# Kernel optimization log

Hardware: AMD Instinct MI355X
Metric: run time of the kernel (lower is better)

## Reference

```python
import jax, jax.numpy as jnp
import numpy as np

N, C, T, V = 64, 64, 256, 25
H, O = 8, 64

def setup_inputs() -> dict:
    key = jax.random.key(0)
    ks = jax.random.split(key, 6)
    s = 0.05
    return {
        "x": jax.random.normal(ks[0], (N, C, T, V), dtype=jnp.float32),
        "A": jax.random.normal(ks[1], (V, V), dtype=jnp.float32) * 0.1,
        "alpha": jnp.float32(1.0),
        "Wq": jax.random.normal(ks[2], (H, C), dtype=jnp.float32) * s,
        "bq": jnp.zeros((H,), dtype=jnp.float32),
        "Wk": jax.random.normal(ks[3], (H, C), dtype=jnp.float32) * s,
        "bk": jnp.zeros((H,), dtype=jnp.float32),
        "Wv": jax.random.normal(ks[4], (O, C), dtype=jnp.float32) * s,
        "bv": jnp.zeros((O,), dtype=jnp.float32),
        "Wr": jax.random.normal(ks[5], (O, H), dtype=jnp.float32) * s,
        "br": jnp.zeros((O,), dtype=jnp.float32),
    }

def reference(x, A, alpha, Wq, bq, Wk, bk, Wv, bv, Wr, br):
    # 1x1 conv projections + temporal mean pooling (bias commutes with mean)
    t = x.shape[2]
    x_mean = x.mean(axis=2)                                   # (N, C, V)
    q = jnp.einsum('ncv,hc->nhv', x_mean, Wq) + bq[None, :, None]   # (N, H, V)
    k = jnp.einsum('ncv,hc->nhv', x_mean, Wk) + bk[None, :, None]   # (N, H, V)
    v = jnp.einsum('nctv,oc->notv', x, Wv) + bv[None, :, None, None]  # (N, O, T, V)
    # outer-difference tanh attention: (N, H, V, V)
    attn = jnp.tanh(q[:, :, :, None] - k[:, :, None, :])
    # 1x1 conv reproject heads -> out channels: (N, O, V, V)
    rep = jnp.einsum('nhuv,oh->nouv', attn, Wr) + br[None, :, None, None]
    masked = alpha * rep + A[None, None, :, :]
    # adjacency-weighted node aggregation
    out = jnp.einsum('ncuv,nctv->nctu', masked, v)            # (N, O, T, V)
    return out
```

## Files before the change

### kernel.cpp

```cpp
#include <hip/hip_runtime.h>
#include <hip/hip_bf16.h>

#define NB 64
#define CC 64
#define TT 256
#define VV 25
#define HH 8
#define OO 64
#define TV (TT*VV)
#define UV (VV*VV)
#define NCHUNK 25

__global__ __launch_bounds__(256) void k_prep(const float* __restrict__ Wv,
                                              float* __restrict__ WvT) {
    int i = blockIdx.x * 256 + threadIdx.x;
    int o = i >> 6, c = i & 63;
    WvT[c * OO + o] = Wv[o * CC + c];
}

__global__ __launch_bounds__(256) void k_vmean(const float* __restrict__ x,
                                               const float* __restrict__ WvT,
                                               const float* __restrict__ bv,
                                               float* __restrict__ vv,
                                               float* __restrict__ xpart) {
    int blk = blockIdx.x;
    int n = blk / NCHUNK, ch = blk % NCHUNK;
    int tid = threadIdx.x;
    int tv = ch * 256 + tid;
    int vloc = tv % VV;

    __shared__ float xacc[CC * VV];
    for (int i = tid; i < CC * VV; i += 256) xacc[i] = 0.0f;
    __syncthreads();

    const float*  xs  = x + (size_t)n * CC * TV + tv;
    const float2* W2  = (const float2*)WvT;
    const float2* bv2 = (const float2*)bv;

    float2 acc[OO / 2];
#pragma unroll
    for (int j = 0; j < OO / 2; ++j) acc[j] = bv2[j];

#pragma unroll 2
    for (int c = 0; c < CC; ++c) {
        float xv = xs[(size_t)c * TV];
        atomicAdd(&xacc[c * VV + vloc], xv);
#pragma unroll
        for (int j = 0; j < OO / 2; ++j) {
            float2 w = W2[c * (OO / 2) + j];
            acc[j].x += w.x * xv;
            acc[j].y += w.y * xv;
        }
    }

    float* dst = vv + (size_t)n * OO * TV + tv;
#pragma unroll
    for (int j = 0; j < OO / 2; ++j) {
        dst[(size_t)(2 * j) * TV]     = acc[j].x;
        dst[(size_t)(2 * j + 1) * TV] = acc[j].y;
    }

    __syncthreads();
    float* xg = xpart + (size_t)blk * (CC * VV);
    for (int i = tid; i < CC * VV; i += 256) xg[i] = xacc[i];
}

__global__ __launch_bounds__(256) void k_masked(
        float* __restrict__ buf,
        const float* __restrict__ A,
        const float* __restrict__ alpha_p,
        const float* __restrict__ Wq, const float* __restrict__ bq,
        const float* __restrict__ Wk, const float* __restrict__ bk,
        const float* __restrict__ Wr, const float* __restrict__ br) {
    int n = blockIdx.x, tid = threadIdx.x;
    __shared__ float xm[CC * VV];
    __shared__ float qs[HH * VV];
    __shared__ float ks[HH * VV];
    __shared__ float attn[HH * UV];

    const float* xp = buf + (size_t)n * (NCHUNK * CC * VV);
    for (int i = tid; i < CC * VV; i += 256) {
        float s = 0.0f;
#pragma unroll
        for (int ch = 0; ch < NCHUNK; ++ch) s += xp[ch * (CC * VV) + i];
        xm[i] = s * (1.0f / TT);
    }
    __syncthreads();

    for (int i = tid; i < 2 * HH * VV; i += 256) {
        int isK = i >= HH * VV;
        int hv = isK ? i - HH * VV : i;
        int h = hv / VV, v = hv % VV;
        const float* W = isK ? Wk : Wq;
        float s = isK ? bk[h] : bq[h];
        for (int c = 0; c < CC; ++c) s += xm[c * VV + v] * W[h * CC + c];
        if (isK) ks[hv] = s; else qs[hv] = s;
    }
    __syncthreads();

    for (int i = tid; i < HH * UV; i += 256) {
        int h = i / UV, uv = i % UV, u = uv / VV, v = uv % VV;
        attn[i] = tanhf(qs[h * VV + u] - ks[h * VV + v]);
    }
    __syncthreads();

    float alpha = alpha_p[0];
    float* mout = buf + (size_t)n * (OO * UV);
    for (int i = tid; i < OO * UV; i += 256) {
        int o = i / UV, uv = i % UV;
        float r = br[o];
#pragma unroll
        for (int h = 0; h < HH; ++h) r += Wr[o * HH + h] * attn[h * UV + uv];
        mout[i] = alpha * r + A[uv];
    }
}

__global__ __launch_bounds__(256) void k_aggr(float* __restrict__ io,
                                              const float* __restrict__ masked) {
    int no = blockIdx.x;
    int t  = threadIdx.x;
    __shared__ float buf[TV];
    float4* b4 = (float4*)buf;
    float4* g4 = (float4*)(io + (size_t)no * TV);

    for (int i = t; i < TV / 4; i += 256) b4[i] = g4[i];
    __syncthreads();

    float xv[VV];
#pragma unroll
    for (int v = 0; v < VV; ++v) xv[v] = buf[t * VV + v];

    const float* m = masked + (size_t)no * UV;
    float outr[VV];
#pragma unroll
    for (int u = 0; u < VV; ++u) {
        float a = 0.0f;
#pragma unroll
        for (int v = 0; v < VV; ++v) a += m[u * VV + v] * xv[v];
        outr[u] = a;
    }
#pragma unroll
    for (int u = 0; u < VV; ++u) buf[t * VV + u] = outr[u];
    __syncthreads();

    for (int i = t; i < TV / 4; i += 256) g4[i] = b4[i];
}

extern "C" void kernel_launch(void* const* d_in, const int* in_sizes, int n_in,
                              void* d_out, int out_size, void* d_ws, size_t ws_size,
                              hipStream_t stream) {
    const float* x     = (const float*)d_in[0];
    const float* A     = (const float*)d_in[1];
    const float* alpha = (const float*)d_in[2];
    const float* Wq    = (const float*)d_in[3];
    const float* bq    = (const float*)d_in[4];
    const float* Wk    = (const float*)d_in[5];
    const float* bk    = (const float*)d_in[6];
    const float* Wv    = (const float*)d_in[7];
    const float* bv    = (const float*)d_in[8];
    const float* Wr    = (const float*)d_in[9];
    const float* br    = (const float*)d_in[10];
    float* out = (float*)d_out;

    float* ws     = (float*)d_ws;
    float* xpart  = ws;
    float* masked = ws;
    float* WvT    = ws + (size_t)NB * OO * UV;

    k_prep  <<<(CC * OO) / 256, 256, 0, stream>>>(Wv, WvT);
    k_vmean <<<NB * NCHUNK, 256, 0, stream>>>(x, WvT, bv, out, xpart);
    k_masked<<<NB, 256, 0, stream>>>(masked, A, alpha, Wq, bq, Wk, bk, Wr, br);
    k_aggr  <<<NB * OO, 256, 0, stream>>>(out, masked);
}
```

Before: 396.6 us.

## Split temporal mean out of V projection into separate reduction kernel

Removes the per-element shared-memory atomicAdd that computed the temporal mean inside the V projection kernel, and puts that mean into its own kernel that reduces each (n,c) slab through shared memory. The V projection now processes four channels per iteration with float4 weight loads and sets a launch-bounds occupancy hint. The cost is a second full read of x (about 105MB) in exchange for cutting LDS atomic contention and the 25-chunk partial-sum buffer.

```diff
diff --git a/kernel.cpp b/kernel.cpp
--- a/kernel.cpp
+++ b/kernel.cpp
@@ -9,7 +9,6 @@
 #define OO 64
 #define TV (TT*VV)
 #define UV (VV*VV)
-#define NCHUNK 25
 
 __global__ __launch_bounds__(256) void k_prep(const float* __restrict__ Wv,
                                               float* __restrict__ WvT) {
@@ -18,73 +17,94 @@
     WvT[c * OO + o] = Wv[o * CC + c];
 }
 
-__global__ __launch_bounds__(256) void k_vmean(const float* __restrict__ x,
-                                               const float* __restrict__ WvT,
-                                               const float* __restrict__ bv,
-                                               float* __restrict__ vv,
-                                               float* __restrict__ xpart) {
+__global__ __launch_bounds__(256, 4) void k_vproj(const float* __restrict__ x,
+                                                  const float* __restrict__ WvT,
+                                                  const float* __restrict__ bv,
+                                                  float* __restrict__ vv) {
     int blk = blockIdx.x;
-    int n = blk / NCHUNK, ch = blk % NCHUNK;
-    int tid = threadIdx.x;
-    int tv = ch * 256 + tid;
-    int vloc = tv % VV;
+    int n = blk / 25, ch = blk % 25;
+    int tv = ch * 256 + threadIdx.x;
 
-    __shared__ float xacc[CC * VV];
-    for (int i = tid; i < CC * VV; i += 256) xacc[i] = 0.0f;
-    __syncthreads();
+    const float*  xs = x + (size_t)n * CC * TV + tv;
+    const float4* W4 = (const float4*)WvT;
+    const float4* b4 = (const float4*)bv;
 
-    const float*  xs  = x + (size_t)n * CC * TV + tv;
-    const float2* W2  = (const float2*)WvT;
-    const float2* bv2 = (const float2*)bv;
+    float4 a[OO / 4];
+#pragma unroll
+    for (int j = 0; j < OO / 4; ++j) a[j] = b4[j];
 
-    float2 acc[OO / 2];
+    for (int c = 0; c < CC; c += 4) {
+        float x0 = xs[(size_t)(c + 0) * TV];
+        float x1 = xs[(size_t)(c + 1) * TV];
+        float x2 = xs[(size_t)(c + 2) * TV];
+        float x3 = xs[(size_t)(c + 3) * TV];
 #pragma unroll
-    for (int j = 0; j < OO / 2; ++j) acc[j] = bv2[j];
-
-#pragma unroll 2
-    for (int c = 0; c < CC; ++c) {
-        float xv = xs[(size_t)c * TV];
-        atomicAdd(&xacc[c * VV + vloc], xv);
-#pragma unroll
-        for (int j = 0; j < OO / 2; ++j) {
-            float2 w = W2[c * (OO / 2) + j];
-            acc[j].x += w.x * xv;
-            acc[j].y += w.y * xv;
+        for (int j = 0; j < OO / 4; ++j) {
+            float4 w0 = W4[(c + 0) * (OO / 4) + j];
+            float4 w1 = W4[(c + 1) * (OO / 4) + j];
+            float4 w2 = W4[(c + 2) * (OO / 4) + j];
+            float4 w3 = W4[(c + 3) * (OO / 4) + j];
+            a[j].x += w0.x * x0; a[j].y += w0.y * x0; a[j].z += w0.z * x0; a[j].w += w0.w * x0;
+            a[j].x += w1.x * x1; a[j].y += w1.y * x1; a[j].z += w1.z * x1; a[j].w += w1.w * x1;
+            a[j].x += w2.x * x2; a[j].y += w2.y * x2; a[j].z += w2.z * x2; a[j].w += w2.w * x2;
+            a[j].x += w3.x * x3; a[j].y += w3.y * x3; a[j].z += w3.z * x3; a[j].w += w3.w * x3;
         }
     }
 
     float* dst = vv + (size_t)n * OO * TV + tv;
 #pragma unroll
-    for (int j = 0; j < OO / 2; ++j) {
-        dst[(size_t)(2 * j) * TV]     = acc[j].x;
-        dst[(size_t)(2 * j + 1) * TV] = acc[j].y;
+    for (int j = 0; j < OO / 4; ++j) {
+        dst[(size_t)(4 * j + 0) * TV] = a[j].x;
+        dst[(size_t)(4 * j + 1) * TV] = a[j].y;
+        dst[(size_t)(4 * j + 2) * TV] = a[j].z;
+        dst[(size_t)(4 * j + 3) * TV] = a[j].w;
     }
+}
 
+__global__ __launch_bounds__(256) void k_mean(const float* __restrict__ x,
+                                              float* __restrict__ xmean) {
+    int nc  = blockIdx.x;
+    int tid = threadIdx.x;
+    __shared__ float tile[TV];
+    __shared__ float part[8 * VV];
+
+    const float4* g4 = (const float4*)(x + (size_t)nc * TV);
+    float4*       t4 = (float4*)tile;
+    for (int i = tid; i < TV / 4; i += 256) t4[i] = g4[i];
     __syncthreads();
-    float* xg = xpart + (size_t)blk * (CC * VV);
-    for (int i = tid; i < CC * VV; i += 256) xg[i] = xacc[i];
+
+    if (tid < 8 * VV) {
+        int g = tid / VV, v = tid % VV;
+        float s = 0.0f;
+#pragma unroll
+        for (int j = 0; j < 32; ++j) s += tile[(g * 32 + j) * VV + v];
+        part[g * VV + v] = s;
+    }
+    __syncthreads();
+
+    if (tid < VV) {
+        float s = 0.0f;
+#pragma unroll
+        for (int g = 0; g < 8; ++g) s += part[g * VV + tid];
+        xmean[(size_t)nc * VV + tid] = s * (1.0f / TT);
+    }
 }
 
 __global__ __launch_bounds__(256) void k_masked(
-        float* __restrict__ buf,
-        const float* __restrict__ A,
+        const float* __restrict__ xmean, const float* __restrict__ A,
         const float* __restrict__ alpha_p,
         const float* __restrict__ Wq, const float* __restrict__ bq,
         const float* __restrict__ Wk, const float* __restrict__ bk,
-        const float* __restrict__ Wr, const float* __restrict__ br) {
+        const float* __restrict__ Wr, const float* __restrict__ br,
+        float* __restrict__ masked) {
     int n = blockIdx.x, tid = threadIdx.x;
     __shared__ float xm[CC * VV];
     __shared__ float qs[HH * VV];
     __shared__ float ks[HH * VV];
     __shared__ float attn[HH * UV];
 
-    const float* xp = buf + (size_t)n * (NCHUNK * CC * VV);
-    for (int i = tid; i < CC * VV; i += 256) {
-        float s = 0.0f;
-#pragma unroll
-        for (int ch = 0; ch < NCHUNK; ++ch) s += xp[ch * (CC * VV) + i];
-        xm[i] = s * (1.0f / TT);
-    }
+    for (int i = tid; i < CC * VV; i += 256)
+        xm[i] = xmean[(size_t)n * CC * VV + i];
     __syncthreads();
 
     for (int i = tid; i < 2 * HH * VV; i += 256) {
@@ -105,13 +125,12 @@
     __syncthreads();
 
     float alpha = alpha_p[0];
-    float* mout = buf + (size_t)n * (OO * UV);
     for (int i = tid; i < OO * UV; i += 256) {
         int o = i / UV, uv = i % UV;
         float r = br[o];
 #pragma unroll
         for (int h = 0; h < HH; ++h) r += Wr[o * HH + h] * attn[h * UV + uv];
-        mout[i] = alpha * r + A[uv];
+        masked[(size_t)n * OO * UV + i] = alpha * r + A[uv];
     }
 }
 
@@ -163,12 +182,13 @@
     float* out = (float*)d_out;
 
     float* ws     = (float*)d_ws;
-    float* xpart  = ws;
     float* masked = ws;
-    float* WvT    = ws + (size_t)NB * OO * UV;
+    float* xmean  = ws + (size_t)NB * OO * UV;
+    float* WvT    = xmean + (size_t)NB * CC * VV;
 
     k_prep  <<<(CC * OO) / 256, 256, 0, stream>>>(Wv, WvT);
-    k_vmean <<<NB * NCHUNK, 256, 0, stream>>>(x, WvT, bv, out, xpart);
-    k_masked<<<NB, 256, 0, stream>>>(masked, A, alpha, Wq, bq, Wk, bk, Wr, br);
+    k_vproj <<<NB * 25, 256, 0, stream>>>(x, WvT, bv, out);
+    k_mean  <<<NB * CC, 256, 0, stream>>>(x, xmean);
+    k_masked<<<NB, 256, 0, stream>>>(xmean, A, alpha, Wq, bq, Wk, bk, Wr, br, masked);
     k_aggr  <<<NB * OO, 256, 0, stream>>>(out, masked);
 }
```

New measurement: 337.8 us. 1.17x faster.
